# Kernel tuning notes

Measured on AMD Instinct MI355X. Metric: run time of the kernel, lower is better.

The kernel has to match this reference:

```python
import jax, jax.numpy as jnp
import numpy as np

N, E, B = 100000, 1200000, 512
IN_DIM, HID, K, NCLS = 64, 64, 3, 10


def setup_inputs() -> dict:
    key = jax.random.key(0)
    ks = jax.random.split(key, 10)
    features = jax.random.normal(ks[0], (N, IN_DIM), jnp.float32)
    edge_src = jax.random.randint(ks[1], (E,), 0, N)
    edge_dst = jax.random.randint(ks[2], (E,), 0, N)
    graph_ids = jnp.sort(jax.random.randint(ks[3], (N,), 0, B))
    s1 = float(1.0 / np.sqrt(IN_DIM))
    W1 = jax.random.uniform(ks[4], (IN_DIM, HID), jnp.float32, -s1, s1)
    b1 = jnp.zeros((HID,), jnp.float32)
    s2 = float(1.0 / np.sqrt(HID))
    W2 = jax.random.uniform(ks[5], (HID, HID), jnp.float32, -s2, s2)
    b2 = jnp.zeros((HID,), jnp.float32)
    s3 = float(1.0 / np.sqrt(HID * 3))
    cw = jax.random.uniform(ks[6], (HID, HID, 3), jnp.float32, -s3, s3)
    cb = jax.random.uniform(ks[7], (HID,), jnp.float32, -s3, s3)
    Wc = jax.random.uniform(ks[8], (HID, NCLS), jnp.float32, -s2, s2)
    bc = jax.random.uniform(ks[9], (NCLS,), jnp.float32, -s2, s2)
    return dict(features=features, edge_src=edge_src, edge_dst=edge_dst,
                graph_ids=graph_ids, num_graphs=B,
                W1=W1, b1=b1, W2=W2, b2=b2, cw=cw, cb=cb, Wc=Wc, bc=bc)


def graph_conv(h, src, dst, W, b, n_nodes):
    # DGL GraphConv, norm='both', allow_zero_in_degree (degrees clamped to 1)
    ones = jnp.ones((src.shape[0],), h.dtype)
    out_deg = jnp.zeros((n_nodes,), h.dtype).at[src].add(ones)
    in_deg = jnp.zeros((n_nodes,), h.dtype).at[dst].add(ones)
    norm_s = jax.lax.rsqrt(jnp.clip(out_deg, 1.0, None))
    norm_d = jax.lax.rsqrt(jnp.clip(in_deg, 1.0, None))
    m = (h * norm_s[:, None]) @ W  # weight first; math identical to agg-first
    agg = jnp.zeros((n_nodes, W.shape[1]), h.dtype).at[dst].add(m[src])
    return agg * norm_d[:, None] + b


def sort_pool(h, gid, num_graphs, k):
    # DGL SortPooling: sort each node's features ascending along feature dim,
    # then take top-k nodes per graph by last feature value (descending),
    # zero-padding graphs with < k nodes. Output [num_graphs, k*D].
    hs = jnp.sort(h, axis=-1)
    key = hs[:, -1]
    order = jnp.lexsort((-key, gid))  # gid asc, key desc
    gid_s = gid[order]
    hs_s = hs[order]
    n = gid.shape[0]
    start = jnp.full((num_graphs,), n).at[gid_s].min(jnp.arange(n))
    rank = jnp.arange(n) - start[gid_s]  # within-graph rank by key desc
    mask = rank < k
    slot = gid_s * k + jnp.clip(rank, 0, k - 1)
    out = jnp.zeros((num_graphs * k, hs.shape[-1]), h.dtype).at[slot].add(
        jnp.where(mask[:, None], hs_s, jnp.zeros((), h.dtype)))
    return out.reshape(num_graphs, k * hs.shape[-1])


def reference(features, edge_src, edge_dst, graph_ids, num_graphs,
              W1, b1, W2, b2, cw, cb, Wc, bc):
    n = features.shape[0]
    h = jax.nn.relu(graph_conv(features, edge_src, edge_dst, W1, b1, n))
    h = jax.nn.relu(graph_conv(h, edge_src, edge_dst, W2, b2, n))
    p = sort_pool(h, graph_ids, num_graphs, K)          # [B, K*HID]
    x = p.reshape(num_graphs, HID, K)                    # faithful torch reshape
    # Conv1d(kernel=3, stride=1) on length-3 input -> length-1 output
    y = jax.nn.relu(jnp.einsum('bct,oct->bo', x, cw) + cb)
    return y @ Wc + bc
```

## Files before the change

### kernel.cpp

```cpp
#include <hip/hip_runtime.h>
#include <hip/hip_bf16.h>


#define PART_H 25088
#define HALF_H (PART_H / 2)
#define PART_F 12544
#define QUART_F (PART_F / 4)
#define MCH  64

__global__ void k_hist1(const int* __restrict__ esrc, const int* __restrict__ edst,
                        unsigned char* __restrict__ hd, unsigned char* __restrict__ hs,
                        int N, int E, int PH) {
  __shared__ unsigned int lc[HALF_H];
  const int b = blockIdx.x;
  const int half = PH * MCH;
  const int a = b / half;
  const int r = b % half;
  const int p = r % PH;
  const int m = r / PH;
  const int* __restrict__ arr = a ? esrc : edst;
  unsigned char* __restrict__ outp = a ? hs : hd;
  const int base = p * PART_H;
  const int lim = min(PART_H, N - base);
  for (int i = threadIdx.x; i < HALF_H; i += blockDim.x) lc[i] = 0u;
  __syncthreads();
  const long long cb = (long long)m * E / MCH;
  const long long ce = (long long)(m + 1) * E / MCH;
  const long long a0 = min((cb + 3) & ~3LL, ce);
  const long long nv = (ce - a0) >> 2;
  for (long long e = cb + threadIdx.x; e < a0; e += blockDim.x) {
    int d = arr[e] - base;
    if ((unsigned)d < (unsigned)lim) atomicAdd(&lc[d >> 1], 1u << ((d & 1) * 16));
  }
  const int4* __restrict__ a4p = (const int4*)(arr + a0);
  for (long long i = threadIdx.x; i < nv; i += blockDim.x) {
    int4 v4 = a4p[i];
    int d;
    d = v4.x - base; if ((unsigned)d < (unsigned)lim) atomicAdd(&lc[d >> 1], 1u << ((d & 1) * 16));
    d = v4.y - base; if ((unsigned)d < (unsigned)lim) atomicAdd(&lc[d >> 1], 1u << ((d & 1) * 16));
    d = v4.z - base; if ((unsigned)d < (unsigned)lim) atomicAdd(&lc[d >> 1], 1u << ((d & 1) * 16));
    d = v4.w - base; if ((unsigned)d < (unsigned)lim) atomicAdd(&lc[d >> 1], 1u << ((d & 1) * 16));
  }
  for (long long e = a0 + (nv << 2) + threadIdx.x; e < ce; e += blockDim.x) {
    int d = arr[e] - base;
    if ((unsigned)d < (unsigned)lim) atomicAdd(&lc[d >> 1], 1u << ((d & 1) * 16));
  }
  __syncthreads();
  unsigned char* slice = outp + ((size_t)p * MCH + m) * PART_H;
  for (int i = threadIdx.x; i < lim; i += blockDim.x)
    slice[i] = (unsigned char)((lc[i >> 1] >> ((i & 1) * 16)) & 0xffffu);
}

__global__ void k_off(unsigned char* __restrict__ hd, const unsigned char* __restrict__ hs,
                      int* __restrict__ deg_d, float* __restrict__ norm_s,
                      float* __restrict__ norm_d, int N) {
  int v = blockIdx.x * blockDim.x + threadIdx.x;
  if (v >= N) return;
  size_t base = (size_t)(v / PART_H) * MCH * PART_H + (v % PART_H);
  int run = 0;
#pragma unroll
  for (int m = 0; m < MCH; ++m) {
    int t = hd[base + (size_t)m * PART_H];
    hd[base + (size_t)m * PART_H] = (unsigned char)run;
    run += t;
  }
  int s = 0;
#pragma unroll
  for (int m = 0; m < MCH; ++m) s += hs[base + (size_t)m * PART_H];
  deg_d[v] = run;
  norm_d[v] = rsqrtf((float)max(run, 1));
  norm_s[v] = rsqrtf((float)max(s, 1));
}

__global__ void k_scan1(const int* __restrict__ deg, int* __restrict__ rowptr,
                        int* __restrict__ bsum, int N) {
  __shared__ int sums[256];
  const int t = threadIdx.x;
  const int base = blockIdx.x * 2048 + t * 8;
  int loc[8];
  int tot = 0;
#pragma unroll
  for (int j = 0; j < 8; ++j) {
    int idx = base + j;
    loc[j] = tot;
    tot += (idx < N) ? deg[idx] : 0;
  }
  sums[t] = tot;
  __syncthreads();
  for (int off = 1; off < 256; off <<= 1) {
    int x = (t >= off) ? sums[t - off] : 0;
    __syncthreads();
    sums[t] += x;
    __syncthreads();
  }
  int excl = (t == 0) ? 0 : sums[t - 1];
#pragma unroll
  for (int j = 0; j < 8; ++j) {
    int idx = base + j;
    if (idx < N) rowptr[idx] = excl + loc[j];
  }
  if (t == 255) bsum[blockIdx.x] = sums[255];
}

__global__ void k_scan2(int* __restrict__ bsum, int nb) {
  int lane = threadIdx.x;
  int v = (lane < nb) ? bsum[lane] : 0;
  int inc = v;
#pragma unroll
  for (int off = 1; off < 64; off <<= 1) {
    int o = __shfl_up(inc, off, 64);
    if (lane >= off) inc += o;
  }
  if (lane < nb) bsum[lane] = inc - v;
}

__global__ void k_scan3(int* __restrict__ rowptr, const int* __restrict__ bsum, int N) {
  int v = blockIdx.x * blockDim.x + threadIdx.x;
  if (v < N) rowptr[v] += bsum[v >> 11];
}

__global__ void k_fill2(const int* __restrict__ esrc, const int* __restrict__ edst,
                        const unsigned char* __restrict__ hd, const int* __restrict__ rowptr,
                        int* __restrict__ csr, int N, int E, int PF) {
  __shared__ unsigned int cur4[QUART_F];
  const int b = blockIdx.x;
  const int p = b % PF;
  const int m = b / PF;
  const int base = p * PART_F;
  const int lim = min(PART_F, N - base);
  const unsigned char* slice = hd + ((size_t)(p >> 1) * MCH + m) * PART_H
                                  + (size_t)(p & 1) * PART_F;
  const unsigned int* slice4 = (const unsigned int*)slice;
  for (int i = threadIdx.x; i < QUART_F; i += blockDim.x) cur4[i] = slice4[i];
  __syncthreads();
  const int* __restrict__ rp = rowptr + base;
  const long long cb = (long long)m * E / MCH;
  const long long ce = (long long)(m + 1) * E / MCH;
  const long long a0 = min((cb + 3) & ~3LL, ce);
  const long long nv = (ce - a0) >> 2;
  for (long long e = cb + threadIdx.x; e < a0; e += blockDim.x) {
    int d = edst[e] - base;
    if ((unsigned)d < (unsigned)lim) {
      unsigned int old = atomicAdd(&cur4[d >> 2], 1u << ((d & 3) * 8));
      int off = (old >> ((d & 3) * 8)) & 0xff;
      csr[rp[d] + off] = esrc[e];
    }
  }
  const int4* __restrict__ d4p = (const int4*)(edst + a0);
  const int4* __restrict__ s4p = (const int4*)(esrc + a0);
  for (long long i = threadIdx.x; i < nv; i += blockDim.x) {
    int4 d4 = d4p[i];
    int4 s4 = s4p[i];
    int d;
    d = d4.x - base;
    if ((unsigned)d < (unsigned)lim) {
      unsigned int old = atomicAdd(&cur4[d >> 2], 1u << ((d & 3) * 8));
      csr[rp[d] + ((old >> ((d & 3) * 8)) & 0xff)] = s4.x;
    }
    d = d4.y - base;
    if ((unsigned)d < (unsigned)lim) {
      unsigned int old = atomicAdd(&cur4[d >> 2], 1u << ((d & 3) * 8));
      csr[rp[d] + ((old >> ((d & 3) * 8)) & 0xff)] = s4.y;
    }
    d = d4.z - base;
    if ((unsigned)d < (unsigned)lim) {
      unsigned int old = atomicAdd(&cur4[d >> 2], 1u << ((d & 3) * 8));
      csr[rp[d] + ((old >> ((d & 3) * 8)) & 0xff)] = s4.z;
    }
    d = d4.w - base;
    if ((unsigned)d < (unsigned)lim) {
      unsigned int old = atomicAdd(&cur4[d >> 2], 1u << ((d & 3) * 8));
      csr[rp[d] + ((old >> ((d & 3) * 8)) & 0xff)] = s4.w;
    }
  }
  for (long long e = a0 + (nv << 2) + threadIdx.x; e < ce; e += blockDim.x) {
    int d = edst[e] - base;
    if ((unsigned)d < (unsigned)lim) {
      unsigned int old = atomicAdd(&cur4[d >> 2], 1u << ((d & 3) * 8));
      csr[rp[d] + ((old >> ((d & 3) * 8)) & 0xff)] = esrc[e];
    }
  }
}

__global__ void __launch_bounds__(256) k_gemm64(
    const float* __restrict__ in, const float* __restrict__ norm,
    const float* __restrict__ W, float* __restrict__ out, int N) {
  __shared__ float Wl[4096];
  __shared__ float Ac[64 * 136];
  const int t = threadIdx.x;
  const int ch = (t & 7) * 8;
  const int nb = (t >> 3) * 4;
  for (int i = t; i < 1024; i += 256)
    ((float4*)Wl)[i] = ((const float4*)W)[i];

  const int NT = (N + 127) >> 7;
  for (int tile = blockIdx.x; tile < NT; tile += gridDim.x) {
    const int vbase = tile << 7;
    __syncthreads();
    for (int i = t; i < 2048; i += 256) {
      const int r = i >> 4;
      const int c = (i & 15) * 4;
      const int v = vbase + r;
      float4 val = make_float4(0.f, 0.f, 0.f, 0.f);
      if (v < N) val = *(const float4*)(in + (size_t)v * 64 + c);
      Ac[(c + 0) * 136 + r] = val.x;
      Ac[(c + 1) * 136 + r] = val.y;
      Ac[(c + 2) * 136 + r] = val.z;
      Ac[(c + 3) * 136 + r] = val.w;
    }
    __syncthreads();

    float acc[4][8];
#pragma unroll
    for (int j = 0; j < 4; ++j)
#pragma unroll
      for (int c = 0; c < 8; ++c) acc[j][c] = 0.f;

    for (int k = 0; k < 64; k += 4) {
#pragma unroll
      for (int kk = 0; kk < 4; ++kk) {
        const float4 aa = *(const float4*)&Ac[(k + kk) * 136 + nb];
        const float4 w0 = *(const float4*)&Wl[(k + kk) * 64 + ch];
        const float4 w1 = *(const float4*)&Wl[(k + kk) * 64 + ch + 4];
        const float an[4] = {aa.x, aa.y, aa.z, aa.w};
        const float wn[8] = {w0.x, w0.y, w0.z, w0.w, w1.x, w1.y, w1.z, w1.w};
#pragma unroll
        for (int j = 0; j < 4; ++j)
#pragma unroll
          for (int c = 0; c < 8; ++c)
            acc[j][c] = fmaf(an[j], wn[c], acc[j][c]);
      }
    }

#pragma unroll
    for (int j = 0; j < 4; ++j) {
      const int v = vbase + nb + j;
      if (v < N) {
        const float nm = norm[v];
        float4 o0, o1;
        o0.x = acc[j][0] * nm; o0.y = acc[j][1] * nm;
        o0.z = acc[j][2] * nm; o0.w = acc[j][3] * nm;
        o1.x = acc[j][4] * nm; o1.y = acc[j][5] * nm;
        o1.z = acc[j][6] * nm; o1.w = acc[j][7] * nm;
        *(float4*)(out + (size_t)v * 64 + ch)     = o0;
        *(float4*)(out + (size_t)v * 64 + ch + 4) = o1;
      }
    }
  }
}

__global__ void k_gather(const float* __restrict__ m, const int* __restrict__ rowptr,
                         const int* __restrict__ deg, const float* __restrict__ norm_d,
                         const float* __restrict__ bias, const int* __restrict__ csr,
                         float* __restrict__ h, float* __restrict__ key, int N) {
  const int w = blockIdx.x * (blockDim.x >> 6) + (threadIdx.x >> 6);
  if (w >= N) return;
  const int lane = threadIdx.x & 63;
  const int quad = lane & 15;
  const int grp = lane >> 4;
  const int start = rowptr[w];
  const int cnt = deg[w];
  float4 acc0 = make_float4(0.f, 0.f, 0.f, 0.f);
  float4 acc1 = make_float4(0.f, 0.f, 0.f, 0.f);
  int i = grp;
  for (; i + 4 < cnt; i += 8) {
    int s0 = csr[start + i];
    int s1 = csr[start + i + 4];
    const float4 v0 = *(const float4*)(m + (size_t)s0 * 64 + quad * 4);
    const float4 v1 = *(const float4*)(m + (size_t)s1 * 64 + quad * 4);
    acc0.x += v0.x; acc0.y += v0.y; acc0.z += v0.z; acc0.w += v0.w;
    acc1.x += v1.x; acc1.y += v1.y; acc1.z += v1.z; acc1.w += v1.w;
  }
  if (i < cnt) {
    int s0 = csr[start + i];
    const float4 v0 = *(const float4*)(m + (size_t)s0 * 64 + quad * 4);
    acc0.x += v0.x; acc0.y += v0.y; acc0.z += v0.z; acc0.w += v0.w;
  }
  acc0.x += acc1.x; acc0.y += acc1.y; acc0.z += acc1.z; acc0.w += acc1.w;
#pragma unroll
  for (int off = 16; off <= 32; off <<= 1) {
    acc0.x += __shfl_xor(acc0.x, off, 64);
    acc0.y += __shfl_xor(acc0.y, off, 64);
    acc0.z += __shfl_xor(acc0.z, off, 64);
    acc0.w += __shfl_xor(acc0.w, off, 64);
  }
  const float nd = norm_d[w];
  const float4 bq = *(const float4*)(bias + quad * 4);
  float4 o;
  o.x = fmaxf(fmaf(acc0.x, nd, bq.x), 0.f);
  o.y = fmaxf(fmaf(acc0.y, nd, bq.y), 0.f);
  o.z = fmaxf(fmaf(acc0.z, nd, bq.z), 0.f);
  o.w = fmaxf(fmaf(acc0.w, nd, bq.w), 0.f);
  if (grp == 0) *(float4*)(h + (size_t)w * 64 + quad * 4) = o;
  if (key != nullptr) {
    float mx = fmaxf(fmaxf(o.x, o.y), fmaxf(o.z, o.w));
#pragma unroll
    for (int off = 1; off < 16; off <<= 1) mx = fmaxf(mx, __shfl_xor(mx, off, 64));
    if (lane == 0) key[w] = mx;
  }
}

__global__ void k_bstart(const int* __restrict__ gid, int* __restrict__ gstart, int N) {
  int i = blockIdx.x * blockDim.x + threadIdx.x;
  if (i >= N) return;
  int g = gid[i];
  if (i == 0 || gid[i - 1] != g) gstart[g] = i;
}

__global__ void k_bfin(const int* __restrict__ gstart, int* __restrict__ gcnt,
                       int B, int N) {
  __shared__ int sm[512];
  const int g = threadIdx.x;
  sm[g] = (g < B) ? gstart[g] : 0x7fffffff;
  __syncthreads();
  for (int off = 1; off < 512; off <<= 1) {
    int x = (g + off < 512) ? sm[g + off] : 0x7fffffff;
    __syncthreads();
    sm[g] = min(sm[g], x);
    __syncthreads();
  }
  if (g < B) {
    int gs = gstart[g];
    int ns = (g + 1 < 512) ? min(sm[g + 1], N) : N;
    gcnt[g] = (gs < N) ? (ns - gs) : 0;
  }
}

__global__ void k_top3(const float* __restrict__ key, const int* __restrict__ gstart,
                       const int* __restrict__ gcnt, int* __restrict__ sel, int B) {
  const int lane = threadIdx.x & 63;
  const int g = blockIdx.x * (blockDim.x >> 6) + (threadIdx.x >> 6);
  if (g >= B) return;
  const int s = gstart[g], c = gcnt[g];
  float v0 = -1.f, v1 = -1.f, v2 = -1.f;
  int i0 = 0x7fffffff, i1 = 0x7fffffff, i2 = 0x7fffffff;
  for (int i = s + lane; i < s + c; i += 64) {
    float kv = key[i];
    if (kv > v0 || (kv == v0 && i < i0)) {
      v2 = v1; i2 = i1; v1 = v0; i1 = i0; v0 = kv; i0 = i;
    } else if (kv > v1 || (kv == v1 && i < i1)) {
      v2 = v1; i2 = i1; v1 = kv; i1 = i;
    } else if (kv > v2 || (kv == v2 && i < i2)) {
      v2 = kv; i2 = i;
    }
  }
  int ptr = 0;
  for (int r = 0; r < 3; ++r) {
    float mv = (ptr == 0) ? v0 : (ptr == 1) ? v1 : (ptr == 2) ? v2 : -1.f;
    int   mi = (ptr == 0) ? i0 : (ptr == 1) ? i1 : (ptr == 2) ? i2 : 0x7fffffff;
    float bv = mv; int bi = mi;
#pragma unroll
    for (int off = 32; off; off >>= 1) {
      float ov = __shfl_xor(bv, off, 64);
      int   oi = __shfl_xor(bi, off, 64);
      if (ov > bv || (ov == bv && oi < bi)) { bv = ov; bi = oi; }
    }
    if (bi == mi && ptr < 3) ptr++;
    if (lane == 0) sel[g * 3 + r] = (bi == 0x7fffffff) ? -1 : bi;
  }
}

__global__ void k_pool(const float* __restrict__ h, const int* __restrict__ sel,
                       float* __restrict__ p, int B) {
  const int lane = threadIdx.x & 63;
  const int w = blockIdx.x * (blockDim.x >> 6) + (threadIdx.x >> 6);
  if (w >= B * 3) return;
  int node = sel[w];
  float v = 0.f;
  if (node >= 0) {
    v = h[(size_t)node * 64 + lane];
    for (int k2 = 2; k2 <= 64; k2 <<= 1) {
      for (int j = k2 >> 1; j > 0; j >>= 1) {
        float o = __shfl_xor(v, j, 64);
        bool up = ((lane & k2) == 0);
        bool lower = ((lane & j) == 0);
        v = (lower == up) ? fminf(v, o) : fmaxf(v, o);
      }
    }
  }
  p[(size_t)w * 64 + lane] = v;
}

__global__ void k_cls(const float* __restrict__ p, const float* __restrict__ cw,
                      const float* __restrict__ cb, const float* __restrict__ Wc,
                      const float* __restrict__ bc, float* __restrict__ out, int B) {
  __shared__ float prow[192];
  const int b = blockIdx.x;
  const int lane = threadIdx.x;
  prow[lane] = p[(size_t)b * 192 + lane];
  prow[lane + 64] = p[(size_t)b * 192 + lane + 64];
  prow[lane + 128] = p[(size_t)b * 192 + lane + 128];
  __syncthreads();
  float y = cb[lane];
  for (int j = 0; j < 192; ++j) y = fmaf(prow[j], cw[lane * 192 + j], y);
  float ry = fmaxf(y, 0.f);
  for (int c = 0; c < 10; ++c) {
    float s = ry * Wc[lane * 10 + c];
#pragma unroll
    for (int off = 32; off; off >>= 1) s += __shfl_xor(s, off, 64);
    if (lane == 0) out[b * 10 + c] = s + bc[c];
  }
}

extern "C" void kernel_launch(void* const* d_in, const int* in_sizes, int n_in,
                              void* d_out, int out_size, void* d_ws, size_t ws_size,
                              hipStream_t stream) {
  const float* features = (const float*)d_in[0];
  const int*   esrc     = (const int*)d_in[1];
  const int*   edst     = (const int*)d_in[2];
  const int*   gid      = (const int*)d_in[3];
  const float* W1 = (const float*)d_in[5];
  const float* b1 = (const float*)d_in[6];
  const float* W2 = (const float*)d_in[7];
  const float* b2 = (const float*)d_in[8];
  const float* cw = (const float*)d_in[9];
  const float* cb = (const float*)d_in[10];
  const float* Wc = (const float*)d_in[11];
  const float* bc = (const float*)d_in[12];
  float* out = (float*)d_out;

  const int N = in_sizes[0] / 64;
  const int E = in_sizes[1];
  const int B = out_size / 10;
  const size_t N64 = (size_t)N * 64;
  const int nscan = (N + 2047) / 2048;
  const int PH = (N + PART_H - 1) / PART_H;
  const int PF = (N + PART_F - 1) / PART_F;
  const size_t HSZ = (size_t)PH * MCH * PART_H;
  const int NT = (N + 127) / 128;

  float* bufA   = (float*)d_ws;
  float* bufB   = bufA + N64;
  int*   deg_d  = (int*)(bufB + N64);
  float* norm_s = (float*)(deg_d + N);
  float* norm_d = norm_s + N;
  float* key    = norm_d + N;
  int*   rowptr = (int*)(key + N);
  int*   csr    = rowptr + N;
  int*   bsum   = csr + E;
  int*   gstart = bsum + 64;
  int*   gcnt   = gstart + B;
  int*   sel    = gcnt + B;
  float* p      = (float*)(sel + 3 * B);
  unsigned char* hd = (unsigned char*)(p + 192 * B);
  unsigned char* hs = hd + HSZ;

  const int TB = 256;

  k_hist1<<<2 * PH * MCH, TB, 0, stream>>>(esrc, edst, hd, hs, N, E, PH);
  k_off<<<(N + TB - 1) / TB, TB, 0, stream>>>(hd, hs, deg_d, norm_s, norm_d, N);
  k_scan1<<<nscan, 256, 0, stream>>>(deg_d, rowptr, bsum, N);
  k_scan2<<<1, 64, 0, stream>>>(bsum, nscan);
  k_scan3<<<(N + TB - 1) / TB, TB, 0, stream>>>(rowptr, bsum, N);
  k_fill2<<<PF * MCH, TB, 0, stream>>>(esrc, edst, hd, rowptr, csr, N, E, PF);

  k_gemm64<<<NT, TB, 0, stream>>>(features, norm_s, W1, bufA, N);
  k_gather<<<(N + 3) / 4, TB, 0, stream>>>(bufA, rowptr, deg_d, norm_d, b1, csr,
                                           bufB, nullptr, N);

  k_gemm64<<<NT, TB, 0, stream>>>(bufB, norm_s, W2, bufA, N);
  k_gather<<<(N + 3) / 4, TB, 0, stream>>>(bufA, rowptr, deg_d, norm_d, b2, csr,
                                           bufB, key, N);

  hipMemsetAsync(gstart, 0x7f, (size_t)B * sizeof(int), stream);
  k_bstart<<<(N + TB - 1) / TB, TB, 0, stream>>>(gid, gstart, N);
  k_bfin<<<1, 512, 0, stream>>>(gstart, gcnt, B, N);
  k_top3<<<(B + 3) / 4, TB, 0, stream>>>(key, gstart, gcnt, sel, B);
  k_pool<<<(B * 3 + 3) / 4, TB, 0, stream>>>(bufB, sel, p, B);

  k_cls<<<B, 64, 0, stream>>>(p, cw, cb, Wc, bc, out, B);
}
```

Before: 328.2 us.

## Co-schedule first GEMM with histogram, fuse graph-start and pooling tail kernels

The first layer's dense transform no longer needs norm_s. It is merged into the degree-histogram launch as extra blocks, and the source normalisation moves into the gather as a per-neighbour scale. Graph-start detection is folded into the second gather, and top-3 selection, feature sort, pooling and the classifier are fused into one per-graph kernel. This removes several kernel launches and lets GEMM work overlap the atomic-bound histogram. The cost is an extra per-edge norm load in the first gather and a larger shared-memory footprint for the histogram blocks.

Result: faster. 307.1 us (-6.4%).

```diff
diff --git a/kernel.cpp b/kernel.cpp
--- a/kernel.cpp
+++ b/kernel.cpp
@@ -8,47 +8,110 @@
 #define QUART_F (PART_F / 4)
 #define MCH  64
 
-__global__ void k_hist1(const int* __restrict__ esrc, const int* __restrict__ edst,
-                        unsigned char* __restrict__ hd, unsigned char* __restrict__ hs,
-                        int N, int E, int PH) {
-  __shared__ unsigned int lc[HALF_H];
-  const int b = blockIdx.x;
-  const int half = PH * MCH;
-  const int a = b / half;
-  const int r = b % half;
-  const int p = r % PH;
-  const int m = r / PH;
-  const int* __restrict__ arr = a ? esrc : edst;
-  unsigned char* __restrict__ outp = a ? hs : hd;
-  const int base = p * PART_H;
-  const int lim = min(PART_H, N - base);
-  for (int i = threadIdx.x; i < HALF_H; i += blockDim.x) lc[i] = 0u;
-  __syncthreads();
-  const long long cb = (long long)m * E / MCH;
-  const long long ce = (long long)(m + 1) * E / MCH;
-  const long long a0 = min((cb + 3) & ~3LL, ce);
-  const long long nv = (ce - a0) >> 2;
-  for (long long e = cb + threadIdx.x; e < a0; e += blockDim.x) {
-    int d = arr[e] - base;
-    if ((unsigned)d < (unsigned)lim) atomicAdd(&lc[d >> 1], 1u << ((d & 1) * 16));
-  }
-  const int4* __restrict__ a4p = (const int4*)(arr + a0);
-  for (long long i = threadIdx.x; i < nv; i += blockDim.x) {
-    int4 v4 = a4p[i];
-    int d;
-    d = v4.x - base; if ((unsigned)d < (unsigned)lim) atomicAdd(&lc[d >> 1], 1u << ((d & 1) * 16));
-    d = v4.y - base; if ((unsigned)d < (unsigned)lim) atomicAdd(&lc[d >> 1], 1u << ((d & 1) * 16));
-    d = v4.z - base; if ((unsigned)d < (unsigned)lim) atomicAdd(&lc[d >> 1], 1u << ((d & 1) * 16));
-    d = v4.w - base; if ((unsigned)d < (unsigned)lim) atomicAdd(&lc[d >> 1], 1u << ((d & 1) * 16));
-  }
-  for (long long e = a0 + (nv << 2) + threadIdx.x; e < ce; e += blockDim.x) {
-    int d = arr[e] - base;
-    if ((unsigned)d < (unsigned)lim) atomicAdd(&lc[d >> 1], 1u << ((d & 1) * 16));
-  }
-  __syncthreads();
-  unsigned char* slice = outp + ((size_t)p * MCH + m) * PART_H;
-  for (int i = threadIdx.x; i < lim; i += blockDim.x)
-    slice[i] = (unsigned char)((lc[i >> 1] >> ((i & 1) * 16)) & 0xffffu);
+__global__ void __launch_bounds__(256) k_histgemm(
+    const int* __restrict__ esrc, const int* __restrict__ edst,
+    unsigned char* __restrict__ hd, unsigned char* __restrict__ hs,
+    const float* __restrict__ in, const float* __restrict__ W,
+    float* __restrict__ mout, int N, int E, int PH, int histBlocks) {
+  __shared__ float smem[12800];
+  const int t = threadIdx.x;
+  if (blockIdx.x < histBlocks) {
+    unsigned int* lc = (unsigned int*)smem;
+    const int b = blockIdx.x;
+    const int half = PH * MCH;
+    const int a = b / half;
+    const int r = b % half;
+    const int p = r % PH;
+    const int m = r / PH;
+    const int* __restrict__ arr = a ? esrc : edst;
+    unsigned char* __restrict__ outp = a ? hs : hd;
+    const int base = p * PART_H;
+    const int lim = min(PART_H, N - base);
+    for (int i = t; i < HALF_H; i += 256) lc[i] = 0u;
+    __syncthreads();
+    const long long cb = (long long)m * E / MCH;
+    const long long ce = (long long)(m + 1) * E / MCH;
+    const long long a0 = min((cb + 3) & ~3LL, ce);
+    const long long nv = (ce - a0) >> 2;
+    for (long long e = cb + t; e < a0; e += 256) {
+      int d = arr[e] - base;
+      if ((unsigned)d < (unsigned)lim) atomicAdd(&lc[d >> 1], 1u << ((d & 1) * 16));
+    }
+    const int4* __restrict__ a4p = (const int4*)(arr + a0);
+    for (long long i = t; i < nv; i += 256) {
+      int4 v4 = a4p[i];
+      int d;
+      d = v4.x - base; if ((unsigned)d < (unsigned)lim) atomicAdd(&lc[d >> 1], 1u << ((d & 1) * 16));
+      d = v4.y - base; if ((unsigned)d < (unsigned)lim) atomicAdd(&lc[d >> 1], 1u << ((d & 1) * 16));
+      d = v4.z - base; if ((unsigned)d < (unsigned)lim) atomicAdd(&lc[d >> 1], 1u << ((d & 1) * 16));
+      d = v4.w - base; if ((unsigned)d < (unsigned)lim) atomicAdd(&lc[d >> 1], 1u << ((d & 1) * 16));
+    }
+    for (long long e = a0 + (nv << 2) + t; e < ce; e += 256) {
+      int d = arr[e] - base;
+      if ((unsigned)d < (unsigned)lim) atomicAdd(&lc[d >> 1], 1u << ((d & 1) * 16));
+    }
+    __syncthreads();
+    unsigned char* slice = outp + ((size_t)p * MCH + m) * PART_H;
+    for (int i = t; i < lim; i += 256)
+      slice[i] = (unsigned char)((lc[i >> 1] >> ((i & 1) * 16)) & 0xffffu);
+  } else {
+    float* Wl = smem;
+    float* Ac = smem + 4096;
+    const int ch = (t & 7) * 8;
+    const int nb = (t >> 3) * 4;
+    for (int i = t; i < 1024; i += 256)
+      ((float4*)Wl)[i] = ((const float4*)W)[i];
+    const int gb = blockIdx.x - histBlocks;
+    const int ng = gridDim.x - histBlocks;
+    const int NT = (N + 127) >> 7;
+    for (int tile = gb; tile < NT; tile += ng) {
+      const int vbase = tile << 7;
+      __syncthreads();
+      for (int i = t; i < 2048; i += 256) {
+        const int r = i >> 4;
+        const int c = (i & 15) * 4;
+        const int v = vbase + r;
+        float4 val = make_float4(0.f, 0.f, 0.f, 0.f);
+        if (v < N) val = *(const float4*)(in + (size_t)v * 64 + c);
+        Ac[(c + 0) * 136 + r] = val.x;
+        Ac[(c + 1) * 136 + r] = val.y;
+        Ac[(c + 2) * 136 + r] = val.z;
+        Ac[(c + 3) * 136 + r] = val.w;
+      }
+      __syncthreads();
+      float acc[4][8];
+#pragma unroll
+      for (int j = 0; j < 4; ++j)
+#pragma unroll
+        for (int c = 0; c < 8; ++c) acc[j][c] = 0.f;
+      for (int k = 0; k < 64; k += 4) {
+#pragma unroll
+        for (int kk = 0; kk < 4; ++kk) {
+          const float4 aa = *(const float4*)&Ac[(k + kk) * 136 + nb];
+          const float4 w0 = *(const float4*)&Wl[(k + kk) * 64 + ch];
+          const float4 w1 = *(const float4*)&Wl[(k + kk) * 64 + ch + 4];
+          const float an[4] = {aa.x, aa.y, aa.z, aa.w};
+          const float wn[8] = {w0.x, w0.y, w0.z, w0.w, w1.x, w1.y, w1.z, w1.w};
+#pragma unroll
+          for (int j = 0; j < 4; ++j)
+#pragma unroll
+            for (int c = 0; c < 8; ++c)
+              acc[j][c] = fmaf(an[j], wn[c], acc[j][c]);
+        }
+      }
+#pragma unroll
+      for (int j = 0; j < 4; ++j) {
+        const int v = vbase + nb + j;
+        if (v < N) {
+          float4 o0, o1;
+          o0.x = acc[j][0]; o0.y = acc[j][1]; o0.z = acc[j][2]; o0.w = acc[j][3];
+          o1.x = acc[j][4]; o1.y = acc[j][5]; o1.z = acc[j][6]; o1.w = acc[j][7];
+          *(float4*)(mout + (size_t)v * 64 + ch)     = o0;
+          *(float4*)(mout + (size_t)v * 64 + ch + 4) = o1;
+        }
+      }
+    }
+  }
 }
 
 __global__ void k_off(unsigned char* __restrict__ hd, const unsigned char* __restrict__ hs,
@@ -142,8 +205,7 @@
     int d = edst[e] - base;
     if ((unsigned)d < (unsigned)lim) {
       unsigned int old = atomicAdd(&cur4[d >> 2], 1u << ((d & 3) * 8));
-      int off = (old >> ((d & 3) * 8)) & 0xff;
-      csr[rp[d] + off] = esrc[e];
+      csr[rp[d] + ((old >> ((d & 3) * 8)) & 0xff)] = esrc[e];
     }
   }
   const int4* __restrict__ d4p = (const int4*)(edst + a0);
@@ -192,7 +254,6 @@
   const int nb = (t >> 3) * 4;
   for (int i = t; i < 1024; i += 256)
     ((float4*)Wl)[i] = ((const float4*)W)[i];
-
   const int NT = (N + 127) >> 7;
   for (int tile = blockIdx.x; tile < NT; tile += gridDim.x) {
     const int vbase = tile << 7;
@@ -209,13 +270,11 @@
       Ac[(c + 3) * 136 + r] = val.w;
     }
     __syncthreads();
-
     float acc[4][8];
 #pragma unroll
     for (int j = 0; j < 4; ++j)
 #pragma unroll
       for (int c = 0; c < 8; ++c) acc[j][c] = 0.f;
-
     for (int k = 0; k < 64; k += 4) {
 #pragma unroll
       for (int kk = 0; kk < 4; ++kk) {
@@ -231,7 +290,6 @@
             acc[j][c] = fmaf(an[j], wn[c], acc[j][c]);
       }
     }
-
 #pragma unroll
     for (int j = 0; j < 4; ++j) {
       const int v = vbase + nb + j;
@@ -252,29 +310,56 @@
 __global__ void k_gather(const float* __restrict__ m, const int* __restrict__ rowptr,
                          const int* __restrict__ deg, const float* __restrict__ norm_d,
                          const float* __restrict__ bias, const int* __restrict__ csr,
+                         const float* __restrict__ nsrc,
+                         const int* __restrict__ gid, int* __restrict__ gstart,
                          float* __restrict__ h, float* __restrict__ key, int N) {
   const int w = blockIdx.x * (blockDim.x >> 6) + (threadIdx.x >> 6);
   if (w >= N) return;
   const int lane = threadIdx.x & 63;
   const int quad = lane & 15;
   const int grp = lane >> 4;
+  if (gid != nullptr && lane == 0) {
+    int g = gid[w];
+    if (w == 0 || gid[w - 1] != g) gstart[g] = w;
+  }
   const int start = rowptr[w];
   const int cnt = deg[w];
   float4 acc0 = make_float4(0.f, 0.f, 0.f, 0.f);
   float4 acc1 = make_float4(0.f, 0.f, 0.f, 0.f);
   int i = grp;
-  for (; i + 4 < cnt; i += 8) {
-    int s0 = csr[start + i];
-    int s1 = csr[start + i + 4];
-    const float4 v0 = *(const float4*)(m + (size_t)s0 * 64 + quad * 4);
-    const float4 v1 = *(const float4*)(m + (size_t)s1 * 64 + quad * 4);
-    acc0.x += v0.x; acc0.y += v0.y; acc0.z += v0.z; acc0.w += v0.w;
-    acc1.x += v1.x; acc1.y += v1.y; acc1.z += v1.z; acc1.w += v1.w;
-  }
-  if (i < cnt) {
-    int s0 = csr[start + i];
-    const float4 v0 = *(const float4*)(m + (size_t)s0 * 64 + quad * 4);
-    acc0.x += v0.x; acc0.y += v0.y; acc0.z += v0.z; acc0.w += v0.w;
+  if (nsrc != nullptr) {
+    for (; i + 4 < cnt; i += 8) {
+      int s0 = csr[start + i];
+      int s1 = csr[start + i + 4];
+      float n0 = nsrc[s0], n1 = nsrc[s1];
+      const float4 v0 = *(const float4*)(m + (size_t)s0 * 64 + quad * 4);
+      const float4 v1 = *(const float4*)(m + (size_t)s1 * 64 + quad * 4);
+      acc0.x = fmaf(v0.x, n0, acc0.x); acc0.y = fmaf(v0.y, n0, acc0.y);
+      acc0.z = fmaf(v0.z, n0, acc0.z); acc0.w = fmaf(v0.w, n0, acc0.w);
+      acc1.x = fmaf(v1.x, n1, acc1.x); acc1.y = fmaf(v1.y, n1, acc1.y);
+      acc1.z = fmaf(v1.z, n1, acc1.z); acc1.w = fmaf(v1.w, n1, acc1.w);
+    }
+    if (i < cnt) {
+      int s0 = csr[start + i];
+      float n0 = nsrc[s0];
+      const float4 v0 = *(const float4*)(m + (size_t)s0 * 64 + quad * 4);
+      acc0.x = fmaf(v0.x, n0, acc0.x); acc0.y = fmaf(v0.y, n0, acc0.y);
+      acc0.z = fmaf(v0.z, n0, acc0.z); acc0.w = fmaf(v0.w, n0, acc0.w);
+    }
+  } else {
+    for (; i + 4 < cnt; i += 8) {
+      int s0 = csr[start + i];
+      int s1 = csr[start + i + 4];
+      const float4 v0 = *(const float4*)(m + (size_t)s0 * 64 + quad * 4);
+      const float4 v1 = *(const float4*)(m + (size_t)s1 * 64 + quad * 4);
+      acc0.x += v0.x; acc0.y += v0.y; acc0.z += v0.z; acc0.w += v0.w;
+      acc1.x += v1.x; acc1.y += v1.y; acc1.z += v1.z; acc1.w += v1.w;
+    }
+    if (i < cnt) {
+      int s0 = csr[start + i];
+      const float4 v0 = *(const float4*)(m + (size_t)s0 * 64 + quad * 4);
+      acc0.x += v0.x; acc0.y += v0.y; acc0.z += v0.z; acc0.w += v0.w;
+    }
   }
   acc0.x += acc1.x; acc0.y += acc1.y; acc0.z += acc1.z; acc0.w += acc1.w;
 #pragma unroll
@@ -300,13 +385,6 @@
   }
 }
 
-__global__ void k_bstart(const int* __restrict__ gid, int* __restrict__ gstart, int N) {
-  int i = blockIdx.x * blockDim.x + threadIdx.x;
-  if (i >= N) return;
-  int g = gid[i];
-  if (i == 0 || gid[i - 1] != g) gstart[g] = i;
-}
-
 __global__ void k_bfin(const int* __restrict__ gstart, int* __restrict__ gcnt,
                        int B, int N) {
   __shared__ int sm[512];
@@ -326,79 +404,75 @@
   }
 }
 
-__global__ void k_top3(const float* __restrict__ key, const int* __restrict__ gstart,
-                       const int* __restrict__ gcnt, int* __restrict__ sel, int B) {
-  const int lane = threadIdx.x & 63;
-  const int g = blockIdx.x * (blockDim.x >> 6) + (threadIdx.x >> 6);
-  if (g >= B) return;
-  const int s = gstart[g], c = gcnt[g];
-  float v0 = -1.f, v1 = -1.f, v2 = -1.f;
-  int i0 = 0x7fffffff, i1 = 0x7fffffff, i2 = 0x7fffffff;
-  for (int i = s + lane; i < s + c; i += 64) {
-    float kv = key[i];
-    if (kv > v0 || (kv == v0 && i < i0)) {
-      v2 = v1; i2 = i1; v1 = v0; i1 = i0; v0 = kv; i0 = i;
-    } else if (kv > v1 || (kv == v1 && i < i1)) {
-      v2 = v1; i2 = i1; v1 = kv; i1 = i;
-    } else if (kv > v2 || (kv == v2 && i < i2)) {
-      v2 = kv; i2 = i;
-    }
-  }
-  int ptr = 0;
-  for (int r = 0; r < 3; ++r) {
-    float mv = (ptr == 0) ? v0 : (ptr == 1) ? v1 : (ptr == 2) ? v2 : -1.f;
-    int   mi = (ptr == 0) ? i0 : (ptr == 1) ? i1 : (ptr == 2) ? i2 : 0x7fffffff;
-    float bv = mv; int bi = mi;
-#pragma unroll
-    for (int off = 32; off; off >>= 1) {
-      float ov = __shfl_xor(bv, off, 64);
-      int   oi = __shfl_xor(bi, off, 64);
-      if (ov > bv || (ov == bv && oi < bi)) { bv = ov; bi = oi; }
-    }
-    if (bi == mi && ptr < 3) ptr++;
-    if (lane == 0) sel[g * 3 + r] = (bi == 0x7fffffff) ? -1 : bi;
-  }
-}
-
-__global__ void k_pool(const float* __restrict__ h, const int* __restrict__ sel,
-                       float* __restrict__ p, int B) {
-  const int lane = threadIdx.x & 63;
-  const int w = blockIdx.x * (blockDim.x >> 6) + (threadIdx.x >> 6);
-  if (w >= B * 3) return;
-  int node = sel[w];
-  float v = 0.f;
-  if (node >= 0) {
-    v = h[(size_t)node * 64 + lane];
-    for (int k2 = 2; k2 <= 64; k2 <<= 1) {
-      for (int j = k2 >> 1; j > 0; j >>= 1) {
-        float o = __shfl_xor(v, j, 64);
-        bool up = ((lane & k2) == 0);
-        bool lower = ((lane & j) == 0);
-        v = (lower == up) ? fminf(v, o) : fmaxf(v, o);
-      }
-    }
-  }
-  p[(size_t)w * 64 + lane] = v;
-}
-
-__global__ void k_cls(const float* __restrict__ p, const float* __restrict__ cw,
-                      const float* __restrict__ cb, const float* __restrict__ Wc,
-                      const float* __restrict__ bc, float* __restrict__ out, int B) {
+__global__ void __launch_bounds__(256) k_tail(
+    const float* __restrict__ key, const int* __restrict__ gstart,
+    const int* __restrict__ gcnt, const float* __restrict__ h,
+    const float* __restrict__ cw, const float* __restrict__ cb,
+    const float* __restrict__ Wc, const float* __restrict__ bc,
+    float* __restrict__ out, int B, int N) {
+  __shared__ int sel[3];
   __shared__ float prow[192];
   const int b = blockIdx.x;
-  const int lane = threadIdx.x;
-  prow[lane] = p[(size_t)b * 192 + lane];
-  prow[lane + 64] = p[(size_t)b * 192 + lane + 64];
-  prow[lane + 128] = p[(size_t)b * 192 + lane + 128];
+  const int wid = threadIdx.x >> 6;
+  const int lane = threadIdx.x & 63;
+
+  if (wid == 0) {
+    const int s = gstart[b], c = gcnt[b];
+    float v0 = -1.f, v1 = -1.f, v2 = -1.f;
+    int i0 = 0x7fffffff, i1 = 0x7fffffff, i2 = 0x7fffffff;
+    for (int i = s + lane; i < s + c; i += 64) {
+      float kv = key[i];
+      if (kv > v0 || (kv == v0 && i < i0)) {
+        v2 = v1; i2 = i1; v1 = v0; i1 = i0; v0 = kv; i0 = i;
+      } else if (kv > v1 || (kv == v1 && i < i1)) {
+        v2 = v1; i2 = i1; v1 = kv; i1 = i;
+      } else if (kv > v2 || (kv == v2 && i < i2)) {
+        v2 = kv; i2 = i;
+      }
+    }
+    int ptr = 0;
+    for (int r = 0; r < 3; ++r) {
+      float mv = (ptr == 0) ? v0 : (ptr == 1) ? v1 : (ptr == 2) ? v2 : -1.f;
+      int   mi = (ptr == 0) ? i0 : (ptr == 1) ? i1 : (ptr == 2) ? i2 : 0x7fffffff;
+      float bv = mv; int bi = mi;
+#pragma unroll
+      for (int off = 32; off; off >>= 1) {
+        float ov = __shfl_xor(bv, off, 64);
+        int   oi = __shfl_xor(bi, off, 64);
+        if (ov > bv || (ov == bv && oi < bi)) { bv = ov; bi = oi; }
+      }
+      if (bi == mi && ptr < 3) ptr++;
+      if (lane == 0) sel[r] = (bi == 0x7fffffff) ? -1 : bi;
+    }
+  }
   __syncthreads();
-  float y = cb[lane];
-  for (int j = 0; j < 192; ++j) y = fmaf(prow[j], cw[lane * 192 + j], y);
-  float ry = fmaxf(y, 0.f);
-  for (int c = 0; c < 10; ++c) {
-    float s = ry * Wc[lane * 10 + c];
-#pragma unroll
-    for (int off = 32; off; off >>= 1) s += __shfl_xor(s, off, 64);
-    if (lane == 0) out[b * 10 + c] = s + bc[c];
+  if (wid < 3) {
+    int node = sel[wid];
+    float v = 0.f;
+    if (node >= 0) {
+      v = h[(size_t)node * 64 + lane];
+      for (int k2 = 2; k2 <= 64; k2 <<= 1) {
+        for (int j = k2 >> 1; j > 0; j >>= 1) {
+          float o = __shfl_xor(v, j, 64);
+          bool up = ((lane & k2) == 0);
+          bool lower = ((lane & j) == 0);
+          v = (lower == up) ? fminf(v, o) : fmaxf(v, o);
+        }
+      }
+    }
+    prow[wid * 64 + lane] = v;
+  }
+  __syncthreads();
+  if (wid == 0) {
+    float y = cb[lane];
+    for (int j = 0; j < 192; ++j) y = fmaf(prow[j], cw[lane * 192 + j], y);
+    float ry = fmaxf(y, 0.f);
+    for (int c = 0; c < 10; ++c) {
+      float s = ry * Wc[lane * 10 + c];
+#pragma unroll
+      for (int off = 32; off; off >>= 1) s += __shfl_xor(s, off, 64);
+      if (lane == 0) out[b * 10 + c] = s + bc[c];
+    }
   }
 }
 
@@ -428,6 +502,7 @@
   const int PF = (N + PART_F - 1) / PART_F;
   const size_t HSZ = (size_t)PH * MCH * PART_H;
   const int NT = (N + 127) / 128;
+  const int histBlocks = 2 * PH * MCH;
 
   float* bufA   = (float*)d_ws;
   float* bufB   = bufA + N64;
@@ -440,33 +515,31 @@
   int*   bsum   = csr + E;
   int*   gstart = bsum + 64;
   int*   gcnt   = gstart + B;
-  int*   sel    = gcnt + B;
-  float* p      = (float*)(sel + 3 * B);
-  unsigned char* hd = (unsigned char*)(p + 192 * B);
+  unsigned char* hd = (unsigned char*)(gcnt + B);
   unsigned char* hs = hd + HSZ;
 
   const int TB = 256;
 
-  k_hist1<<<2 * PH * MCH, TB, 0, stream>>>(esrc, edst, hd, hs, N, E, PH);
+  hipMemsetAsync(gstart, 0x7f, (size_t)B * sizeof(int), stream);
+
+  k_histgemm<<<histBlocks + NT, TB, 0, stream>>>(esrc, edst, hd, hs,
+                                                 features, W1, bufA,
+                                                 N, E, PH, histBlocks);
   k_off<<<(N + TB - 1) / TB, TB, 0, stream>>>(hd, hs, deg_d, norm_s, norm_d, N);
   k_scan1<<<nscan, 256, 0, stream>>>(deg_d, rowptr, bsum, N);
   k_scan2<<<1, 64, 0, stream>>>(bsum, nscan);
   k_scan3<<<(N + TB - 1) / TB, TB, 0, stream>>>(rowptr, bsum, N);
   k_fill2<<<PF * MCH, TB, 0, stream>>>(esrc, edst, hd, rowptr, csr, N, E, PF);
 
-  k_gemm64<<<NT, TB, 0, stream>>>(features, norm_s, W1, bufA, N);
   k_gather<<<(N + 3) / 4, TB, 0, stream>>>(bufA, rowptr, deg_d, norm_d, b1, csr,
+                                           norm_s, nullptr, nullptr,
                                            bufB, nullptr, N);
 
   k_gemm64<<<NT, TB, 0, stream>>>(bufB, norm_s, W2, bufA, N);
   k_gather<<<(N + 3) / 4, TB, 0, stream>>>(bufA, rowptr, deg_d, norm_d, b2, csr,
+                                           nullptr, gid, gstart,
                                            bufB, key, N);
 
-  hipMemsetAsync(gstart, 0x7f, (size_t)B * sizeof(int), stream);
-  k_bstart<<<(N + TB - 1) / TB, TB, 0, stream>>>(gid, gstart, N);
   k_bfin<<<1, 512, 0, stream>>>(gstart, gcnt, B, N);
-  k_top3<<<(B + 3) / 4, TB, 0, stream>>>(key, gstart, gcnt, sel, B);
-  k_pool<<<(B * 3 + 3) / 4, TB, 0, stream>>>(bufB, sel, p, B);
-
-  k_cls<<<B, 64, 0, stream>>>(p, cw, cb, Wc, bc, out, B);
-}
+  k_tail<<<B, TB, 0, stream>>>(key, gstart, gcnt, bufB, cw, cb, Wc, bc, out, B, N);
+}
```
